# Optimization experiments

Measured on AMD Instinct MI355X. Metric: run time of the kernel, lower is better.

Reference implementation:

```python
import jax, jax.numpy as jnp
import numpy as np

NUM_CLASSES = 81
NEG_POS_RATIO = 3
LOC_WEIGHT = 1.0
CONF_WEIGHT = 1.0

B, P = 32, 32768


def setup_inputs() -> dict:
    key = jax.random.key(0)
    k1, k2, k3, k4 = jax.random.split(key, 4)
    loc_data = jax.random.normal(k1, (B, P, 4), dtype=jnp.float32)
    conf_data = jax.random.normal(k2, (B, P, NUM_CLASSES), dtype=jnp.float32)
    loc_t = jax.random.normal(k3, (B, P, 4), dtype=jnp.float32)
    conf_t = jax.random.randint(k4, (B, P), 0, NUM_CLASSES, dtype=jnp.int32)
    return {"loc_data": loc_data, "conf_data": conf_data, "loc_t": loc_t, "conf_t": conf_t}


def _smooth_l1(pred, tgt):
    d = pred - tgt
    ad = jnp.abs(d)
    return jnp.where(ad < 1.0, 0.5 * d * d, ad - 0.5)


def reference(loc_data, conf_data, loc_t, conf_t):
    num_priors = loc_data.shape[1]
    pos = conf_t > 0  # [B, P]

    # localization loss: smooth-L1 summed over positive priors
    loss_l = jnp.sum(_smooth_l1(loc_data, loc_t) * pos[..., None].astype(loc_data.dtype))

    # per-prior cross entropy: log_sum_exp(conf) - conf[label] == -log_softmax[label]
    logp = jax.nn.log_softmax(conf_data, axis=-1)  # [B, P, C]
    ce = -jnp.take_along_axis(logp, conf_t[..., None].astype(jnp.int32), axis=-1)[..., 0]  # [B, P]

    # hard negative mining: rank negatives by CE loss (positives zeroed out)
    loss_mine = jnp.where(pos, 0.0, ce)
    loss_idx = jnp.argsort(-loss_mine, axis=1)          # descending sort indices
    idx_rank = jnp.argsort(loss_idx, axis=1)            # rank of each prior
    num_pos = jnp.sum(pos.astype(jnp.int32), axis=1, keepdims=True)  # [B, 1]
    num_neg = jnp.minimum(NEG_POS_RATIO * num_pos, num_priors - 1)
    neg = idx_rank < num_neg                            # [B, P]

    sel = jnp.logical_or(pos, neg)
    loss_c = jnp.sum(jnp.where(sel, ce, 0.0))

    N = jnp.sum(num_pos).astype(loc_data.dtype)
    return (loss_l / N * LOC_WEIGHT, loss_c / N * CONF_WEIGHT)
```

## Files before the change

### kernel.cpp

```cpp
#include <hip/hip_runtime.h>

#define BB 32
#define PP 32768
#define CC 81
#define RPB 64
#define TPB 256
#define NT 16
#define GRID ((BB * PP) / (RPB * NT))


__device__ __forceinline__ float sl1f(float d) {
    float ad = fabsf(d);
    return ad < 1.f ? 0.5f * d * d : ad - 0.5f;
}

#define EXP4(w) { w.x = __expf(w.x); w.y = __expf(w.y); w.z = __expf(w.z); w.w = __expf(w.w); }

__global__ __launch_bounds__(TPB) void ce_loc_kernel(
    const float* __restrict__ conf, const int* __restrict__ labels,
    const float* __restrict__ locd, const float* __restrict__ loct,
    float* __restrict__ mine, double* __restrict__ d_ll, double* __restrict__ d_ce,
    double* __restrict__ d_msum, int* __restrict__ num_pos, int* __restrict__ nnz)
{
    __shared__ float ex[RPB * CC];
    __shared__ float part[4][5];

    const int t = threadIdx.x;
    const int r = t >> 2, q = t & 3;
    const size_t row0 = (size_t)blockIdx.x * (RPB * NT);
    const int b = blockIdx.x >> 5;

    float4 v0, v1, v2, v3, v4, vt;
    {
        const float4* s = (const float4*)(conf + row0 * CC);
        v0 = s[t]; v1 = s[t + 256]; v2 = s[t + 512]; v3 = s[t + 768]; v4 = s[t + 1024];
        if (t < 16) vt = s[1280 + t];
    }

    float a_ll = 0.f, a_pce = 0.f, a_pc = 0.f, a_mv = 0.f, a_nz = 0.f;

    for (int it = 0; it < NT; ++it) {
        __syncthreads();
        float4* dx = (float4*)ex;
        float4 w;
        w = v0; EXP4(w); dx[t]        = w;
        w = v1; EXP4(w); dx[t + 256]  = w;
        w = v2; EXP4(w); dx[t + 512]  = w;
        w = v3; EXP4(w); dx[t + 768]  = w;
        w = v4; EXP4(w); dx[t + 1024] = w;
        if (t < 16) { w = vt; EXP4(w); dx[1280 + t] = w; }

        if (it + 1 < NT) {
            const float4* s = (const float4*)(conf + (row0 + (size_t)(it + 1) * RPB) * CC);
            v0 = s[t]; v1 = s[t + 256]; v2 = s[t + 512]; v3 = s[t + 768]; v4 = s[t + 1024];
            if (t < 16) vt = s[1280 + t];
        }
        __syncthreads();

        const size_t gp = row0 + (size_t)it * RPB + r;
        const int lab = labels[gp];
        const bool pos = lab > 0;
        const float* rowp = ex + r * CC;

        float s0 = 0.f, s1 = 0.f;
#pragma unroll
        for (int c = 0; c < 10; ++c) { s0 += rowp[q + 8 * c]; s1 += rowp[q + 8 * c + 4]; }
        float s = s0 + s1;
        if (q == 0) s += rowp[80];

        float ll = pos ? sl1f(locd[gp * 4 + q] - loct[gp * 4 + q]) : 0.f;

        s  += __shfl_xor(s, 1);  ll += __shfl_xor(ll, 1);
        s  += __shfl_xor(s, 2);  ll += __shfl_xor(ll, 2);

        if (q == 0) {
            const float exl = rowp[lab];
            const float ce = __logf(__fdividef(s, exl));
            a_ll += ll;
            float mv = 0.f;
            if (pos) { a_pce += ce; a_pc += 1.f; }
            else {
                mv = fmaxf(ce, 0.f);
                a_mv += mv;
                a_nz += (mv > 0.f) ? 1.f : 0.f;
            }
            mine[gp] = mv;
        }
    }

#pragma unroll
    for (int off = 32; off; off >>= 1) {
        a_ll  += __shfl_down(a_ll, off);
        a_pce += __shfl_down(a_pce, off);
        a_pc  += __shfl_down(a_pc, off);
        a_mv  += __shfl_down(a_mv, off);
        a_nz  += __shfl_down(a_nz, off);
    }
    const int wv = t >> 6;
    if ((t & 63) == 0) {
        part[wv][0] = a_ll; part[wv][1] = a_pce; part[wv][2] = a_pc;
        part[wv][3] = a_mv; part[wv][4] = a_nz;
    }
    __syncthreads();
    if (t == 0) {
        float x0 = 0, x1 = 0, x2 = 0, x3 = 0, x4 = 0;
#pragma unroll
        for (int i = 0; i < 4; ++i) {
            x0 += part[i][0]; x1 += part[i][1]; x2 += part[i][2];
            x3 += part[i][3]; x4 += part[i][4];
        }
        atomicAdd(&d_ll[b], (double)x0);
        atomicAdd(&d_ce[b], (double)x1);
        atomicAdd(&num_pos[b], (int)x2);
        atomicAdd(&d_msum[b], (double)x3);
        atomicAdd(&nnz[b], (int)x4);
    }
}

__global__ __launch_bounds__(1024) void mine_kernel(
    const float* __restrict__ mine, const int* __restrict__ num_pos,
    const int* __restrict__ nnz, const double* __restrict__ d_msum,
    double* __restrict__ neg_acc)
{
    const int b = blockIdx.x;
    const int t = threadIdx.x;
    const int np = num_pos[b];
    const int k = min(3 * np, PP - 1);
    if (k <= 0) return;

    if (k >= nnz[b]) {
        if (t == 0) atomicAdd(neg_acc, d_msum[b]);
        return;
    }

    const float* mr = mine + (size_t)b * PP;
    __shared__ unsigned hist[256];
    __shared__ unsigned sh_prefix;
    __shared__ int sh_remaining;
    __shared__ float sred[16];

    unsigned prefix = 0;
    int remaining = k;
    for (int lvl = 0; lvl < 4; ++lvl) {
        const int shift = 24 - lvl * 8;
        if (t < 256) hist[t] = 0;
        __syncthreads();
        for (int p = t; p < PP; p += 1024) {
            const unsigned key = __float_as_uint(mr[p]);
            const bool cand = (lvl == 0) || ((key >> (shift + 8)) == prefix);
            const unsigned long long zb = __ballot(cand && key == 0u);
            if ((t & 63) == 0 && zb) atomicAdd(&hist[0], (unsigned)__popcll(zb));
            if (cand && key != 0u) atomicAdd(&hist[(key >> shift) & 255u], 1u);
        }
        __syncthreads();
        if (t == 0) {
            unsigned c = 0;
            int j = 255;
            for (; j > 0; --j) {
                const unsigned h = hist[j];
                if (c + h >= (unsigned)remaining) break;
                c += h;
            }
            sh_prefix = (prefix << 8) | (unsigned)j;
            sh_remaining = remaining - (int)c;
        }
        __syncthreads();
        prefix = sh_prefix;
        remaining = sh_remaining;
        __syncthreads();
    }

    const unsigned vkey = prefix;
    const float v = __uint_as_float(vkey);
    float sgt = 0.f;
    for (int p = t; p < PP; p += 1024) {
        const float mv = mr[p];
        if (__float_as_uint(mv) > vkey) sgt += mv;
    }
#pragma unroll
    for (int off = 32; off; off >>= 1) sgt += __shfl_down(sgt, off);
    if ((t & 63) == 0) sred[t >> 6] = sgt;
    __syncthreads();
    if (t == 0) {
        float tot = 0.f;
#pragma unroll
        for (int w2 = 0; w2 < 16; ++w2) tot += sred[w2];
        tot += (float)remaining * v;
        atomicAdd(neg_acc, (double)tot);
    }
}

__global__ void finalize_kernel(const double* __restrict__ neg_acc,
                                const double* __restrict__ d_ll,
                                const double* __restrict__ d_ce,
                                const int* __restrict__ num_pos,
                                float* __restrict__ out)
{
    if (threadIdx.x == 0 && blockIdx.x == 0) {
        int N = 0;
        double sll = 0.0, sce = 0.0;
#pragma unroll
        for (int b = 0; b < BB; ++b) { N += num_pos[b]; sll += d_ll[b]; sce += d_ce[b]; }
        const double dN = (double)N;
        out[0] = (float)(sll / dN);
        out[1] = (float)((sce + neg_acc[0]) / dN);
    }
}

extern "C" void kernel_launch(void* const* d_in, const int* in_sizes, int n_in,
                              void* d_out, int out_size, void* d_ws, size_t ws_size,
                              hipStream_t stream)
{
    const float* locd   = (const float*)d_in[0];
    const float* conf   = (const float*)d_in[1];
    const float* loct   = (const float*)d_in[2];
    const int*   labels = (const int*)d_in[3];
    float* out = (float*)d_out;

    char* ws = (char*)d_ws;
    double* neg_acc = (double*)ws;
    double* d_ll    = (double*)(ws + 8);
    double* d_ce    = (double*)(ws + 264);
    double* d_msum  = (double*)(ws + 520);
    int*    numpos  = (int*)(ws + 776);
    int*    nnzp    = (int*)(ws + 904);
    float*  mine    = (float*)(ws + 2048);

    hipMemsetAsync(d_ws, 0, 2048, stream);

    ce_loc_kernel<<<GRID, TPB, 0, stream>>>(conf, labels, locd, loct,
                                            mine, d_ll, d_ce, d_msum,
                                            numpos, nnzp);
    mine_kernel<<<BB, 1024, 0, stream>>>(mine, numpos, nnzp, d_msum, neg_acc);
    finalize_kernel<<<1, 64, 0, stream>>>(neg_acc, d_ll, d_ce, numpos, out);
}
```

Measured before the change: 90.10 us.

## Double-buffer conf prefetch and fold finalize into last-block epilogues

The CE kernel now double-buffers its register prefetch: two sets hold the next tile's logits, labels and loc values, so loads for tile i+1 are issued before tile i is exponentiated and reduced. It also sets a min-blocks-per-SM launch bound. The separate finalize kernel is removed. The last CE block computes the final outputs and sets a flag that lets the mining kernel exit early when no top-k selection is needed, and otherwise the last mining block writes the classification loss. This cuts one launch and hides load latency, at the cost of more registers and extra atomics and fences.

New measurement: 291.8 us. 224% more time.

```diff
diff --git a/kernel.cpp b/kernel.cpp
--- a/kernel.cpp
+++ b/kernel.cpp
@@ -16,76 +16,89 @@
 
 #define EXP4(w) { w.x = __expf(w.x); w.y = __expf(w.y); w.z = __expf(w.z); w.w = __expf(w.w); }
 
-__global__ __launch_bounds__(TPB) void ce_loc_kernel(
+#define PREFETCH(SET, IT1) { \
+    const size_t gpn = row0 + (size_t)(IT1) * RPB + r; \
+    lab##SET = labels[gpn]; la##SET = locd[gpn * 4 + q]; lb##SET = loct[gpn * 4 + q]; \
+    const float4* sp = (const float4*)(conf + (row0 + (size_t)(IT1) * RPB) * CC); \
+    v##SET##0 = sp[t];        v##SET##1 = sp[t + 256]; v##SET##2 = sp[t + 512]; \
+    v##SET##3 = sp[t + 768];  v##SET##4 = sp[t + 1024]; \
+    if (t < 16) v##SET##t = sp[1280 + t]; }
+
+#define DEPOSIT(SET) { \
+    float4* dx = (float4*)ex; float4 w; \
+    w = v##SET##0; EXP4(w); dx[t]        = w; \
+    w = v##SET##1; EXP4(w); dx[t + 256]  = w; \
+    w = v##SET##2; EXP4(w); dx[t + 512]  = w; \
+    w = v##SET##3; EXP4(w); dx[t + 768]  = w; \
+    w = v##SET##4; EXP4(w); dx[t + 1024] = w; \
+    if (t < 16) { w = v##SET##t; EXP4(w); dx[1280 + t] = w; } }
+
+#define REDUCE(SET, IT) { \
+    const size_t gp = row0 + (size_t)(IT) * RPB + r; \
+    const bool pos = lab##SET > 0; \
+    const float* rowp = ex + r * CC; \
+    float s0 = 0.f, s1 = 0.f; \
+    _Pragma("unroll") \
+    for (int c = 0; c < 10; ++c) { s0 += rowp[q + 8 * c]; s1 += rowp[q + 8 * c + 4]; } \
+    float s = s0 + s1; \
+    if (q == 0) s += rowp[80]; \
+    float ll = pos ? sl1f(la##SET - lb##SET) : 0.f; \
+    s += __shfl_xor(s, 1);  ll += __shfl_xor(ll, 1); \
+    s += __shfl_xor(s, 2);  ll += __shfl_xor(ll, 2); \
+    if (q == 0) { \
+        const float exl = rowp[lab##SET]; \
+        const float ce = __logf(__fdividef(s, exl)); \
+        a_ll += ll; \
+        float mv = 0.f; \
+        if (pos) { a_pce += ce; a_pc += 1.f; } \
+        else { mv = fmaxf(ce, 0.f); a_mv += mv; a_nz += (mv > 0.f) ? 1.f : 0.f; } \
+        mine[gp] = mv; \
+    } }
+
+__global__ __launch_bounds__(TPB, 4) void ce_loc_kernel(
     const float* __restrict__ conf, const int* __restrict__ labels,
     const float* __restrict__ locd, const float* __restrict__ loct,
-    float* __restrict__ mine, double* __restrict__ d_ll, double* __restrict__ d_ce,
-    double* __restrict__ d_msum, int* __restrict__ num_pos, int* __restrict__ nnz)
+    char* __restrict__ wsb, float* __restrict__ out)
 {
+    int*    done1   = (int*)wsb;
+    int*    flag    = (int*)(wsb + 4);
+    unsigned long long* g_sce = (unsigned long long*)(wsb + 16);
+    unsigned long long* g_N   = (unsigned long long*)(wsb + 24);
+    double* d_ll    = (double*)(wsb + 40);
+    double* d_ce    = (double*)(wsb + 296);
+    double* d_msum  = (double*)(wsb + 552);
+    int*    num_pos = (int*)(wsb + 808);
+    int*    nnz     = (int*)(wsb + 936);
+    float*  mine    = (float*)(wsb + 2048);
+
     __shared__ float ex[RPB * CC];
     __shared__ float part[4][5];
+    __shared__ int lastblk;
 
     const int t = threadIdx.x;
     const int r = t >> 2, q = t & 3;
     const size_t row0 = (size_t)blockIdx.x * (RPB * NT);
     const int b = blockIdx.x >> 5;
 
-    float4 v0, v1, v2, v3, v4, vt;
-    {
-        const float4* s = (const float4*)(conf + row0 * CC);
-        v0 = s[t]; v1 = s[t + 256]; v2 = s[t + 512]; v3 = s[t + 768]; v4 = s[t + 1024];
-        if (t < 16) vt = s[1280 + t];
-    }
+    int labA, labB; float laA, lbA, laB, lbB;
+    float4 vA0, vA1, vA2, vA3, vA4, vAt;
+    float4 vB0, vB1, vB2, vB3, vB4, vBt;
+
+    PREFETCH(A, 0)
 
     float a_ll = 0.f, a_pce = 0.f, a_pc = 0.f, a_mv = 0.f, a_nz = 0.f;
 
-    for (int it = 0; it < NT; ++it) {
-        __syncthreads();
-        float4* dx = (float4*)ex;
-        float4 w;
-        w = v0; EXP4(w); dx[t]        = w;
-        w = v1; EXP4(w); dx[t + 256]  = w;
-        w = v2; EXP4(w); dx[t + 512]  = w;
-        w = v3; EXP4(w); dx[t + 768]  = w;
-        w = v4; EXP4(w); dx[t + 1024] = w;
-        if (t < 16) { w = vt; EXP4(w); dx[1280 + t] = w; }
-
-        if (it + 1 < NT) {
-            const float4* s = (const float4*)(conf + (row0 + (size_t)(it + 1) * RPB) * CC);
-            v0 = s[t]; v1 = s[t + 256]; v2 = s[t + 512]; v3 = s[t + 768]; v4 = s[t + 1024];
-            if (t < 16) vt = s[1280 + t];
-        }
-        __syncthreads();
-
-        const size_t gp = row0 + (size_t)it * RPB + r;
-        const int lab = labels[gp];
-        const bool pos = lab > 0;
-        const float* rowp = ex + r * CC;
-
-        float s0 = 0.f, s1 = 0.f;
-#pragma unroll
-        for (int c = 0; c < 10; ++c) { s0 += rowp[q + 8 * c]; s1 += rowp[q + 8 * c + 4]; }
-        float s = s0 + s1;
-        if (q == 0) s += rowp[80];
-
-        float ll = pos ? sl1f(locd[gp * 4 + q] - loct[gp * 4 + q]) : 0.f;
-
-        s  += __shfl_xor(s, 1);  ll += __shfl_xor(ll, 1);
-        s  += __shfl_xor(s, 2);  ll += __shfl_xor(ll, 2);
-
-        if (q == 0) {
-            const float exl = rowp[lab];
-            const float ce = __logf(__fdividef(s, exl));
-            a_ll += ll;
-            float mv = 0.f;
-            if (pos) { a_pce += ce; a_pc += 1.f; }
-            else {
-                mv = fmaxf(ce, 0.f);
-                a_mv += mv;
-                a_nz += (mv > 0.f) ? 1.f : 0.f;
-            }
-            mine[gp] = mv;
-        }
+    for (int itp = 0; itp < NT / 2; ++itp) {
+        __syncthreads();
+        PREFETCH(B, 2 * itp + 1)
+        DEPOSIT(A)
+        __syncthreads();
+        REDUCE(A, 2 * itp)
+        __syncthreads();
+        if (itp < NT / 2 - 1) PREFETCH(A, 2 * itp + 2)
+        DEPOSIT(B)
+        __syncthreads();
+        REDUCE(B, 2 * itp + 1)
     }
 
 #pragma unroll
@@ -115,95 +128,145 @@
         atomicAdd(&d_msum[b], (double)x3);
         atomicAdd(&nnz[b], (int)x4);
     }
+
+    __threadfence();
+    if (t == 0) lastblk = (atomicAdd(done1, 1) == GRID - 1);
+    __syncthreads();
+    if (!lastblk) return;
+
+    if (t < 64) {
+        double ll = 0.0, ce = 0.0, msel = 0.0;
+        int np = 0, fastf = 1;
+        if (t < 32) {
+            ll = atomicAdd(&d_ll[t], 0.0);
+            ce = atomicAdd(&d_ce[t], 0.0);
+            const double ms = atomicAdd(&d_msum[t], 0.0);
+            np = atomicAdd(&num_pos[t], 0);
+            const int nz = atomicAdd(&nnz[t], 0);
+            const int k = min(3 * np, PP - 1);
+            if (k <= 0)       { fastf = 1; msel = 0.0; }
+            else if (k >= nz) { fastf = 1; msel = ms; }
+            else              { fastf = 0; msel = 0.0; }
+        }
+#pragma unroll
+        for (int off = 32; off; off >>= 1) {
+            ll   += __shfl_down(ll, off);
+            ce   += __shfl_down(ce, off);
+            msel += __shfl_down(msel, off);
+            np   += __shfl_down(np, off);
+            fastf = min(fastf, __shfl_down(fastf, off));
+        }
+        if (t == 0) {
+            const double N = (double)np;
+            out[0] = (float)(ll / N);
+            atomicExch(g_sce, (unsigned long long)__double_as_longlong(ce));
+            atomicExch(g_N,   (unsigned long long)__double_as_longlong(N));
+            if (fastf) {
+                out[1] = (float)((ce + msel) / N);
+                atomicExch(flag, 1);
+            } else {
+                atomicExch(flag, 2);
+            }
+        }
+    }
 }
 
 __global__ __launch_bounds__(1024) void mine_kernel(
-    const float* __restrict__ mine, const int* __restrict__ num_pos,
-    const int* __restrict__ nnz, const double* __restrict__ d_msum,
-    double* __restrict__ neg_acc)
+    char* __restrict__ wsb, float* __restrict__ out)
 {
+    int*    flag    = (int*)(wsb + 4);
+    int*    done2   = (int*)(wsb + 8);
+    unsigned long long* g_sce = (unsigned long long*)(wsb + 16);
+    unsigned long long* g_N   = (unsigned long long*)(wsb + 24);
+    double* neg_acc = (double*)(wsb + 32);
+    double* d_msum  = (double*)(wsb + 552);
+    int*    num_pos = (int*)(wsb + 808);
+    int*    nnz     = (int*)(wsb + 936);
+    const float* mine = (const float*)(wsb + 2048);
+
     const int b = blockIdx.x;
     const int t = threadIdx.x;
-    const int np = num_pos[b];
-    const int k = min(3 * np, PP - 1);
-    if (k <= 0) return;
-
-    if (k >= nnz[b]) {
-        if (t == 0) atomicAdd(neg_acc, d_msum[b]);
-        return;
-    }
-
-    const float* mr = mine + (size_t)b * PP;
-    __shared__ unsigned hist[256];
-    __shared__ unsigned sh_prefix;
-    __shared__ int sh_remaining;
-    __shared__ float sred[16];
-
-    unsigned prefix = 0;
-    int remaining = k;
-    for (int lvl = 0; lvl < 4; ++lvl) {
-        const int shift = 24 - lvl * 8;
-        if (t < 256) hist[t] = 0;
-        __syncthreads();
-        for (int p = t; p < PP; p += 1024) {
-            const unsigned key = __float_as_uint(mr[p]);
-            const bool cand = (lvl == 0) || ((key >> (shift + 8)) == prefix);
-            const unsigned long long zb = __ballot(cand && key == 0u);
-            if ((t & 63) == 0 && zb) atomicAdd(&hist[0], (unsigned)__popcll(zb));
-            if (cand && key != 0u) atomicAdd(&hist[(key >> shift) & 255u], 1u);
-        }
-        __syncthreads();
-        if (t == 0) {
-            unsigned c = 0;
-            int j = 255;
-            for (; j > 0; --j) {
-                const unsigned h = hist[j];
-                if (c + h >= (unsigned)remaining) break;
-                c += h;
-            }
-            sh_prefix = (prefix << 8) | (unsigned)j;
-            sh_remaining = remaining - (int)c;
-        }
-        __syncthreads();
-        prefix = sh_prefix;
-        remaining = sh_remaining;
-        __syncthreads();
-    }
-
-    const unsigned vkey = prefix;
-    const float v = __uint_as_float(vkey);
-    float sgt = 0.f;
-    for (int p = t; p < PP; p += 1024) {
-        const float mv = mr[p];
-        if (__float_as_uint(mv) > vkey) sgt += mv;
-    }
-#pragma unroll
-    for (int off = 32; off; off >>= 1) sgt += __shfl_down(sgt, off);
-    if ((t & 63) == 0) sred[t >> 6] = sgt;
+
+    __shared__ int sh_flag, sh_np, sh_nz;
+    if (t == 0) {
+        sh_flag = atomicAdd(flag, 0);
+        sh_np = atomicAdd(&num_pos[b], 0);
+        sh_nz = atomicAdd(&nnz[b], 0);
+    }
     __syncthreads();
+    if (sh_flag == 1) return;
+
+    const int k = min(3 * sh_np, PP - 1);
+    if (k > 0) {
+        if (k >= sh_nz) {
+            if (t == 0) atomicAdd(neg_acc, atomicAdd(&d_msum[b], 0.0));
+        } else {
+            const float* mr = mine + (size_t)b * PP;
+            __shared__ unsigned hist[256];
+            __shared__ unsigned sh_prefix;
+            __shared__ int sh_remaining;
+            __shared__ float sred[16];
+
+            unsigned prefix = 0;
+            int remaining = k;
+            for (int lvl = 0; lvl < 4; ++lvl) {
+                const int shift = 24 - lvl * 8;
+                if (t < 256) hist[t] = 0;
+                __syncthreads();
+                for (int p = t; p < PP; p += 1024) {
+                    const unsigned key = __float_as_uint(mr[p]);
+                    const bool cand = (lvl == 0) || ((key >> (shift + 8)) == prefix);
+                    const unsigned long long zb = __ballot(cand && key == 0u);
+                    if ((t & 63) == 0 && zb) atomicAdd(&hist[0], (unsigned)__popcll(zb));
+                    if (cand && key != 0u) atomicAdd(&hist[(key >> shift) & 255u], 1u);
+                }
+                __syncthreads();
+                if (t == 0) {
+                    unsigned c = 0;
+                    int j = 255;
+                    for (; j > 0; --j) {
+                        const unsigned h = hist[j];
+                        if (c + h >= (unsigned)remaining) break;
+                        c += h;
+                    }
+                    sh_prefix = (prefix << 8) | (unsigned)j;
+                    sh_remaining = remaining - (int)c;
+                }
+                __syncthreads();
+                prefix = sh_prefix;
+                remaining = sh_remaining;
+                __syncthreads();
+            }
+
+            const unsigned vkey = prefix;
+            const float v = __uint_as_float(vkey);
+            float sgt = 0.f;
+            for (int p = t; p < PP; p += 1024) {
+                const float mv = mr[p];
+                if (__float_as_uint(mv) > vkey) sgt += mv;
+            }
+#pragma unroll
+            for (int off = 32; off; off >>= 1) sgt += __shfl_down(sgt, off);
+            if ((t & 63) == 0) sred[t >> 6] = sgt;
+            __syncthreads();
+            if (t == 0) {
+                float tot = 0.f;
+#pragma unroll
+                for (int w2 = 0; w2 < 16; ++w2) tot += sred[w2];
+                tot += (float)remaining * v;
+                atomicAdd(neg_acc, (double)tot);
+            }
+        }
+    }
+
+    __threadfence();
     if (t == 0) {
-        float tot = 0.f;
-#pragma unroll
-        for (int w2 = 0; w2 < 16; ++w2) tot += sred[w2];
-        tot += (float)remaining * v;
-        atomicAdd(neg_acc, (double)tot);
-    }
-}
-
-__global__ void finalize_kernel(const double* __restrict__ neg_acc,
-                                const double* __restrict__ d_ll,
-                                const double* __restrict__ d_ce,
-                                const int* __restrict__ num_pos,
-                                float* __restrict__ out)
-{
-    if (threadIdx.x == 0 && blockIdx.x == 0) {
-        int N = 0;
-        double sll = 0.0, sce = 0.0;
-#pragma unroll
-        for (int b = 0; b < BB; ++b) { N += num_pos[b]; sll += d_ll[b]; sce += d_ce[b]; }
-        const double dN = (double)N;
-        out[0] = (float)(sll / dN);
-        out[1] = (float)((sce + neg_acc[0]) / dN);
+        if (atomicAdd(done2, 1) == BB - 1) {
+            const double sce = __longlong_as_double((long long)atomicAdd(g_sce, 0ull));
+            const double N   = __longlong_as_double((long long)atomicAdd(g_N, 0ull));
+            const double na  = atomicAdd(neg_acc, 0.0);
+            out[1] = (float)((sce + na) / N);
+        }
     }
 }
 
@@ -216,21 +279,10 @@
     const float* loct   = (const float*)d_in[2];
     const int*   labels = (const int*)d_in[3];
     float* out = (float*)d_out;
-
-    char* ws = (char*)d_ws;
-    double* neg_acc = (double*)ws;
-    double* d_ll    = (double*)(ws + 8);
-    double* d_ce    = (double*)(ws + 264);
-    double* d_msum  = (double*)(ws + 520);
-    int*    numpos  = (int*)(ws + 776);
-    int*    nnzp    = (int*)(ws + 904);
-    float*  mine    = (float*)(ws + 2048);
+    char* wsb = (char*)d_ws;
 
     hipMemsetAsync(d_ws, 0, 2048, stream);
 
-    ce_loc_kernel<<<GRID, TPB, 0, stream>>>(conf, labels, locd, loct,
-                                            mine, d_ll, d_ce, d_msum,
-                                            numpos, nnzp);
-    mine_kernel<<<BB, 1024, 0, stream>>>(mine, numpos, nnzp, d_msum, neg_acc);
-    finalize_kernel<<<1, 64, 0, stream>>>(neg_acc, d_ll, d_ce, numpos, out);
-}
+    ce_loc_kernel<<<GRID, TPB, 0, stream>>>(conf, labels, locd, loct, wsb, out);
+    mine_kernel<<<BB, 1024, 0, stream>>>(wsb, out);
+}
```
